# Performance work log

Measured on AMD Instinct MI355X. Metric: run time of the kernel, lower is better.

## Reference

```python
import jax, jax.numpy as jnp
import numpy as np

N = 50000      # nodes
E = 800000     # edges (before self-loops)
IN_C = 128
H_C = 64
HEADS = 4
OUT_C = 16
NEG_SLOPE = 0.2  # PyG GATConv default


def setup_inputs() -> dict:
    key = jax.random.key(0)
    ks = jax.random.split(key, 11)
    x = jax.random.normal(ks[0], (N, IN_C), dtype=jnp.float32)
    edge_index = jax.random.randint(ks[1], (2, E), 0, N, dtype=jnp.int64)
    def p(k, shape, fan_in):
        return jax.random.normal(k, shape, dtype=jnp.float32) / np.sqrt(fan_in)
    return {
        "x": x,
        "edge_index": edge_index,
        "W1": p(ks[2], (IN_C, HEADS * H_C), IN_C),
        "att_src1": p(ks[3], (HEADS, H_C), H_C),
        "att_dst1": p(ks[4], (HEADS, H_C), H_C),
        "b1": jnp.zeros((HEADS * H_C,), dtype=jnp.float32),
        "W2": p(ks[5], (HEADS * H_C, OUT_C), HEADS * H_C),
        "att_src2": p(ks[6], (1, OUT_C), OUT_C),
        "att_dst2": p(ks[7], (1, OUT_C), OUT_C),
        "b2": jnp.zeros((OUT_C,), dtype=jnp.float32),
    }


def _gat_layer(x, src, dst, W, a_src, a_dst, b, concat):
    n = x.shape[0]
    heads, C = a_src.shape
    h = (x @ W).reshape(n, heads, C)                      # [N,H,C]
    al_s = jnp.einsum('nhc,hc->nh', h, a_src)             # [N,H]
    al_d = jnp.einsum('nhc,hc->nh', h, a_dst)
    e = jax.nn.leaky_relu(al_s[src] + al_d[dst], NEG_SLOPE)  # [E,H]
    # segment softmax over destination neighborhoods
    m = jax.lax.stop_gradient(jax.ops.segment_max(e, dst, num_segments=n))
    p = jnp.exp(e - m[dst])
    denom = jax.ops.segment_sum(p, dst, num_segments=n)
    alpha = p / (denom[dst] + 1e-16)                      # [E,H]
    out = jax.ops.segment_sum(alpha[:, :, None] * h[src], dst, num_segments=n)  # [N,H,C]
    out = out.reshape(n, heads * C) if concat else out.mean(axis=1)
    return out + b


def reference(x, edge_index, W1, att_src1, att_dst1, b1, W2, att_src2, att_dst2, b2):
    # PyG GATConv add_self_loops=True
    loop = jnp.arange(N, dtype=edge_index.dtype)
    src = jnp.concatenate([edge_index[0], loop])
    dst = jnp.concatenate([edge_index[1], loop])
    h = jax.nn.relu(_gat_layer(x, src, dst, W1, att_src1, att_dst1, b1, True))
    out = _gat_layer(h, src, dst, W2, att_src2, att_dst2, b2, False)
    return jax.nn.log_softmax(out, axis=-1)
```

## Files before the change

kernel.cpp:

```cpp
#include <hip/hip_runtime.h>
#include <hip/hip_fp16.h>
#include <cstdint>
#include <cstddef>

#define NEG 0.2f

typedef _Float16 f16x8 __attribute__((ext_vector_type(8)));
typedef float f32x4 __attribute__((ext_vector_type(4)));

__device__ inline float lrelu(float v) { return v > 0.f ? v : NEG * v; }

__global__ void k_pre(const int* __restrict__ ei, int* __restrict__ deg,
                      const float* __restrict__ W1, f16x8* __restrict__ W1s,
                      int E, int ET) {
  int e = blockIdx.x * 256 + threadIdx.x;
  if (e < ET) {
    int d = (e < E) ? ei[E + e] : e - E;
    atomicAdd(&deg[d], 1);
  }
  if (blockIdx.x < 16) {
    int tau = blockIdx.x * 256 + threadIdx.x;
    int l = tau & 63, ct = (tau >> 6) & 15, ks = tau >> 10;
    int col = ct * 16 + (l & 15);
    f16x8 v;
    #pragma unroll
    for (int j = 0; j < 8; j++) {
      int k = ks * 32 + ((j < 4) ? ((l >> 4) * 4 + j) : (16 + (l >> 4) * 4 + (j - 4)));
      v[j] = (_Float16)W1[k * 256 + col];
    }
    W1s[tau] = v;
  }
}

__global__ __launch_bounds__(256) void k_gemm1f(const float* __restrict__ X,
                                                const f16x8* __restrict__ W1s,
                                                const float* __restrict__ as1,
                                                const float* __restrict__ ad1,
                                                __half* __restrict__ H16,
                                                float* __restrict__ als,
                                                float* __restrict__ ald, int N) {
  __shared__ __align__(16) char lds[32768];
  _Float16* A = (_Float16*)lds;
  int t = threadIdx.x;
  int rb = blockIdx.x * 64;
  int l = t & 63, wv = t >> 6;

  #pragma unroll
  for (int i = 0; i < 8; i++) {
    int idx = i * 256 + t;
    int row = idx >> 5, q = idx & 31;
    int gr = rb + row; if (gr >= N) gr = N - 1;
    float4 xv = *(const float4*)(X + (size_t)gr * 128 + q * 4);
    int ks = q >> 3, g = q & 3, hg = (q >> 2) & 1;
    int gran = (ks * 4 + g) ^ (row & 7);
    _Float16* dst = A + row * 128 + gran * 8 + hg * 4;
    dst[0] = (_Float16)xv.x; dst[1] = (_Float16)xv.y;
    dst[2] = (_Float16)xv.z; dst[3] = (_Float16)xv.w;
  }
  __syncthreads();

  f32x4 acc[4][4] = {};
  #pragma unroll
  for (int ks = 0; ks < 4; ks++) {
    f16x8 bfr[4];
    #pragma unroll
    for (int ct = 0; ct < 4; ct++)
      bfr[ct] = W1s[(ks * 16 + wv * 4 + ct) * 64 + l];
    #pragma unroll
    for (int rt = 0; rt < 4; rt++) {
      int row = rt * 16 + (l & 15);
      int gran = (ks * 4 + (l >> 4)) ^ (row & 7);
      f16x8 afr = *(const f16x8*)(A + row * 128 + gran * 8);
      #pragma unroll
      for (int ct = 0; ct < 4; ct++)
        acc[rt][ct] = __builtin_amdgcn_mfma_f32_16x16x32_f16(afr, bfr[ct], acc[rt][ct], 0, 0, 0);
    }
  }

  float asv[4], adv[4];
  #pragma unroll
  for (int ct = 0; ct < 4; ct++) {
    asv[ct] = as1[wv * 64 + ct * 16 + (l & 15)];
    adv[ct] = ad1[wv * 64 + ct * 16 + (l & 15)];
  }
  #pragma unroll
  for (int rt = 0; rt < 4; rt++) {
    #pragma unroll
    for (int j = 0; j < 4; j++) {
      float ps = 0.f, pd = 0.f;
      #pragma unroll
      for (int ct = 0; ct < 4; ct++) {
        ps += acc[rt][ct][j] * asv[ct];
        pd += acc[rt][ct][j] * adv[ct];
      }
      ps += __shfl_xor(ps, 1); ps += __shfl_xor(ps, 2);
      ps += __shfl_xor(ps, 4); ps += __shfl_xor(ps, 8);
      pd += __shfl_xor(pd, 1); pd += __shfl_xor(pd, 2);
      pd += __shfl_xor(pd, 4); pd += __shfl_xor(pd, 8);
      if ((l & 15) == 0) {
        int gr = rb + rt * 16 + (l >> 4) * 4 + j;
        if (gr < N) { als[gr * 4 + wv] = ps; ald[gr * 4 + wv] = pd; }
      }
    }
  }

  __syncthreads();
  _Float16* HL = (_Float16*)lds;
  #pragma unroll
  for (int rt = 0; rt < 4; rt++) {
    #pragma unroll
    for (int j = 0; j < 4; j++) {
      int row = rt * 16 + (l >> 4) * 4 + j;
      #pragma unroll
      for (int ct = 0; ct < 4; ct++) {
        int col = wv * 64 + ct * 16 + (l & 15);
        int g2 = (col >> 3) ^ ((row & 7) << 2);
        HL[row * 256 + g2 * 8 + (col & 7)] = (_Float16)acc[rt][ct][j];
      }
    }
  }
  __syncthreads();
  #pragma unroll
  for (int i = 0; i < 8; i++) {
    int idx = i * 256 + t;
    int row = idx >> 5, g = idx & 31;
    int g2 = g ^ ((row & 7) << 2);
    f32x4 v = *(const f32x4*)(HL + row * 256 + g2 * 8);
    int gr = rb + row;
    if (gr < N) *(f32x4*)((char*)H16 + (size_t)gr * 512 + g * 16) = v;
  }
}

__global__ __launch_bounds__(256) void k_scan_partial(const int* __restrict__ deg,
                                                      int* __restrict__ bsum, int N) {
  __shared__ int sd[256];
  int t = threadIdx.x;
  int base = blockIdx.x * 1024 + t * 4;
  int s = 0;
  #pragma unroll
  for (int j = 0; j < 4; j++) { int i = base + j; s += (i < N) ? deg[i] : 0; }
  sd[t] = s;
  __syncthreads();
  for (int o = 128; o > 0; o >>= 1) {
    if (t < o) sd[t] += sd[t + o];
    __syncthreads();
  }
  if (t == 0) bsum[blockIdx.x] = sd[0];
}

__global__ __launch_bounds__(256) void k_scan_final(const int* __restrict__ deg,
                                                    const int* __restrict__ bsum,
                                                    int* __restrict__ offsets,
                                                    int* __restrict__ cursor,
                                                    int N, int NB) {
  __shared__ int sd[256];
  __shared__ int boffs;
  int b = blockIdx.x, t = threadIdx.x;
  if (t == 0) {
    int r = 0;
    for (int i = 0; i < b; i++) r += bsum[i];
    boffs = r;
  }
  int base = b * 1024 + t * 4;
  int v[4]; int s = 0;
  #pragma unroll
  for (int j = 0; j < 4; j++) { int i = base + j; v[j] = (i < N) ? deg[i] : 0; s += v[j]; }
  int my = s;
  sd[t] = s;
  __syncthreads();
  for (int o = 1; o < 256; o <<= 1) {
    int add = (t >= o) ? sd[t - o] : 0;
    __syncthreads();
    sd[t] += add;
    __syncthreads();
  }
  int run = sd[t] - my + boffs;
  #pragma unroll
  for (int j = 0; j < 4; j++) {
    int i = base + j;
    if (i < N) { offsets[i] = run; cursor[i] = run; run += v[j]; }
  }
  if (b == NB - 1 && t == 255) offsets[N] = boffs + sd[255];
}

__global__ void k_fill(const int* __restrict__ ei, int* __restrict__ cursor,
                       int* __restrict__ csr_src, int E, int ET) {
  int e = blockIdx.x * 256 + threadIdx.x;
  if (e >= ET) return;
  int s, d;
  if (e < E) { s = ei[e]; d = ei[E + e]; } else { s = d = e - E; }
  int pos = atomicAdd(&cursor[d], 1);
  csr_src[pos] = s;
}

__device__ inline void acc8(float4 v, float p, float* a, float& s) {
  __half2 h0 = __builtin_bit_cast(__half2, v.x);
  __half2 h1 = __builtin_bit_cast(__half2, v.y);
  __half2 h2 = __builtin_bit_cast(__half2, v.z);
  __half2 h3 = __builtin_bit_cast(__half2, v.w);
  float2 f0 = __half22float2(h0), f1 = __half22float2(h1);
  float2 f2 = __half22float2(h2), f3 = __half22float2(h3);
  a[0] += p * f0.x; a[1] += p * f0.y; a[2] += p * f1.x; a[3] += p * f1.y;
  a[4] += p * f2.x; a[5] += p * f2.y; a[6] += p * f3.x; a[7] += p * f3.y;
  s += p;
}

__global__ __launch_bounds__(256) void k_agg1(const int* __restrict__ off,
                                              const int* __restrict__ csr_src,
                                              const float* __restrict__ als1,
                                              const float* __restrict__ ald1,
                                              const float4* __restrict__ H16,
                                              const float* __restrict__ b1,
                                              __half* __restrict__ H2, int N) {
  int t = threadIdx.x;
  int n = blockIdx.x * 4 + (t >> 6);
  if (n >= N) return;
  int lane = t & 31;
  int half = (t >> 5) & 1;
  int g = lane >> 3;
  float aldn = ald1[n * 4 + g];
  int st0 = off[n], en0 = off[n + 1];
  int mid = (st0 + en0 + 1) >> 1;
  int st = half ? mid : st0;
  int en = half ? en0 : mid;
  float a[8] = {0.f, 0.f, 0.f, 0.f, 0.f, 0.f, 0.f, 0.f};
  float s = 0.f;
  int i = st;
  for (; i + 4 <= en; i += 4) {
    int s0 = csr_src[i], s1 = csr_src[i + 1], s2 = csr_src[i + 2], s3 = csr_src[i + 3];
    float p0 = __expf(lrelu(als1[s0 * 4 + g] + aldn));
    float p1 = __expf(lrelu(als1[s1 * 4 + g] + aldn));
    float p2 = __expf(lrelu(als1[s2 * 4 + g] + aldn));
    float p3 = __expf(lrelu(als1[s3 * 4 + g] + aldn));
    float4 v0 = H16[(size_t)s0 * 32 + lane];
    float4 v1 = H16[(size_t)s1 * 32 + lane];
    float4 v2 = H16[(size_t)s2 * 32 + lane];
    float4 v3 = H16[(size_t)s3 * 32 + lane];
    acc8(v0, p0, a, s); acc8(v1, p1, a, s); acc8(v2, p2, a, s); acc8(v3, p3, a, s);
  }
  for (; i < en; i++) {
    int s0 = csr_src[i];
    float p0 = __expf(lrelu(als1[s0 * 4 + g] + aldn));
    float4 v0 = H16[(size_t)s0 * 32 + lane];
    acc8(v0, p0, a, s);
  }
  #pragma unroll
  for (int j = 0; j < 8; j++) a[j] += __shfl_xor(a[j], 32);
  s += __shfl_xor(s, 32);
  if (half == 0) {
    float inv = 1.f / (s + 1e-16f);
    int c0 = lane * 8;
    float4 bb0 = *(const float4*)(b1 + c0);
    float4 bb1 = *(const float4*)(b1 + c0 + 4);
    f16x8 o;
    o[0] = (_Float16)fmaxf(a[0] * inv + bb0.x, 0.f);
    o[1] = (_Float16)fmaxf(a[1] * inv + bb0.y, 0.f);
    o[2] = (_Float16)fmaxf(a[2] * inv + bb0.z, 0.f);
    o[3] = (_Float16)fmaxf(a[3] * inv + bb0.w, 0.f);
    o[4] = (_Float16)fmaxf(a[4] * inv + bb1.x, 0.f);
    o[5] = (_Float16)fmaxf(a[5] * inv + bb1.y, 0.f);
    o[6] = (_Float16)fmaxf(a[6] * inv + bb1.z, 0.f);
    o[7] = (_Float16)fmaxf(a[7] * inv + bb1.w, 0.f);
    *(f16x8*)((char*)H2 + (size_t)n * 512 + lane * 16) = o;
  }
}

__global__ __launch_bounds__(256) void k_gemm2(const __half* __restrict__ H2,
                                               const float* __restrict__ W2,
                                               const float* __restrict__ as2,
                                               const float* __restrict__ ad2,
                                               float* __restrict__ Z,
                                               float* __restrict__ als2,
                                               float* __restrict__ ald2, int N) {
  __shared__ float w2s[4096];
  int t = threadIdx.x;
  for (int i = t; i < 4096; i += 256) w2s[i] = W2[i];
  __syncthreads();
  int n = blockIdx.x * 16 + (t >> 4);
  int c = t & 15;
  if (n >= N) return;
  const f16x8* hp = (const f16x8*)((const char*)H2 + (size_t)n * 512);
  float acc = 0.f;
  #pragma unroll 8
  for (int kb = 0; kb < 32; kb++) {
    f16x8 hv = hp[kb];
    #pragma unroll
    for (int j = 0; j < 8; j++)
      acc += (float)hv[j] * w2s[(kb * 8 + j) * 16 + c];
  }
  Z[(size_t)n * 16 + c] = acc;
  float ps = acc * as2[c], pd = acc * ad2[c];
  #pragma unroll
  for (int o = 8; o > 0; o >>= 1) {
    ps += __shfl_down(ps, o, 16);
    pd += __shfl_down(pd, o, 16);
  }
  if (c == 0) { als2[n] = ps; ald2[n] = pd; }
}

__global__ __launch_bounds__(256) void k_agg2x(const int* __restrict__ off,
                                               const int* __restrict__ csr_src,
                                               const float* __restrict__ als2,
                                               const float* __restrict__ ald2,
                                               const float* __restrict__ Z,
                                               const float* __restrict__ b2,
                                               float* __restrict__ out, int N) {
  int t = threadIdx.x;
  int n = blockIdx.x * 8 + (t >> 5);
  if (n >= N) return;
  int c = t & 15;
  int half = (t >> 4) & 1;
  float aldn = ald2[n];
  int st0 = off[n], en0 = off[n + 1];
  int mid = (st0 + en0 + 1) >> 1;
  int st = half ? mid : st0;
  int en = half ? en0 : mid;
  float s = 0.f, acc = 0.f;
  int i = st;
  for (; i + 4 <= en; i += 4) {
    int s0 = csr_src[i], s1 = csr_src[i + 1], s2 = csr_src[i + 2], s3 = csr_src[i + 3];
    float p0 = __expf(lrelu(als2[s0] + aldn));
    float p1 = __expf(lrelu(als2[s1] + aldn));
    float p2 = __expf(lrelu(als2[s2] + aldn));
    float p3 = __expf(lrelu(als2[s3] + aldn));
    float z0 = Z[(size_t)s0 * 16 + c];
    float z1 = Z[(size_t)s1 * 16 + c];
    float z2 = Z[(size_t)s2 * 16 + c];
    float z3 = Z[(size_t)s3 * 16 + c];
    acc += p0 * z0 + p1 * z1 + p2 * z2 + p3 * z3;
    s += p0 + p1 + p2 + p3;
  }
  for (; i < en; i++) {
    int s0 = csr_src[i];
    float p0 = __expf(lrelu(als2[s0] + aldn));
    acc += p0 * Z[(size_t)s0 * 16 + c];
    s += p0;
  }
  acc += __shfl_xor(acc, 16);
  s += __shfl_xor(s, 16);
  if (half == 0) {
    float v = acc / (s + 1e-16f) + b2[c];
    float mx = v;
    #pragma unroll
    for (int o = 8; o > 0; o >>= 1) mx = fmaxf(mx, __shfl_xor(mx, o, 16));
    float ex = __expf(v - mx);
    float sm = ex;
    #pragma unroll
    for (int o = 8; o > 0; o >>= 1) sm += __shfl_xor(sm, o, 16);
    out[(size_t)n * 16 + c] = v - mx - logf(sm);
  }
}

extern "C" void kernel_launch(void* const* d_in, const int* in_sizes, int n_in,
                              void* d_out, int out_size, void* d_ws, size_t ws_size,
                              hipStream_t stream) {
  const float* x   = (const float*)d_in[0];
  const int*   ei  = (const int*)d_in[1];
  const float* W1  = (const float*)d_in[2];
  const float* as1 = (const float*)d_in[3];
  const float* ad1 = (const float*)d_in[4];
  const float* b1  = (const float*)d_in[5];
  const float* W2  = (const float*)d_in[6];
  const float* as2 = (const float*)d_in[7];
  const float* ad2 = (const float*)d_in[8];
  const float* b2  = (const float*)d_in[9];
  float* out = (float*)d_out;

  int N  = in_sizes[0] / 128;
  int E  = in_sizes[1] / 2;
  int ET = E + N;
  int NB = (N + 1023) / 1024;

  char* w = (char*)d_ws;
  size_t off_b = 0;
  auto alloc = [&](size_t bytes) -> char* {
    size_t start = (off_b + 255) & ~(size_t)255;
    off_b = start + bytes;
    return w + start;
  };
  __half*   h16  = (__half*)alloc((size_t)N * 256 * 2);
  __half*   h2   = (__half*)alloc((size_t)N * 256 * 2);
  f16x8*    w1s  = (f16x8*)alloc((size_t)4096 * 16);
  float*    als1 = (float*)alloc((size_t)N * 4 * 4);
  float*    ald1 = (float*)alloc((size_t)N * 4 * 4);
  int*      deg  = (int*)alloc((size_t)N * 4);
  int*      offs = (int*)alloc((size_t)(N + 1) * 4);
  int*      cur  = (int*)alloc((size_t)N * 4);
  int*      bsum = (int*)alloc((size_t)NB * 4);
  int*      csrs = (int*)alloc((size_t)ET * 4);
  float*    z    = (float*)alloc((size_t)N * 16 * 4);
  float*    als2 = (float*)alloc((size_t)N * 4);
  float*    ald2 = (float*)alloc((size_t)N * 4);

  hipMemsetAsync(deg, 0, (size_t)N * 4, stream);

  k_pre<<<(ET + 255) / 256, 256, 0, stream>>>(ei, deg, W1, w1s, E, ET);
  k_gemm1f<<<(N + 63) / 64, 256, 0, stream>>>(x, w1s, as1, ad1, h16, als1, ald1, N);
  k_scan_partial<<<NB, 256, 0, stream>>>(deg, bsum, N);
  k_scan_final<<<NB, 256, 0, stream>>>(deg, bsum, offs, cur, N, NB);
  k_fill<<<(ET + 255) / 256, 256, 0, stream>>>(ei, cur, csrs, E, ET);
  k_agg1<<<(N + 3) / 4, 256, 0, stream>>>(offs, csrs, als1, ald1, (const float4*)h16, b1, h2, N);
  k_gemm2<<<(N + 15) / 16, 256, 0, stream>>>(h2, W2, as2, ad2, z, als2, ald2, N);
  k_agg2x<<<(N + 7) / 8, 256, 0, stream>>>(offs, csrs, als2, ald2, z, b2, out, N);
}
```

Baseline: 233.1 us.

## Fuse CSR build phases into one cooperative kernel with grid syncs

Replaces the memset, degree count, W1 swizzle, two scan kernels and the CSR fill with a single cooperative kernel of 1024 blocks that uses grid-wide syncs between phases. This removes several kernel launches and their gaps. In exchange it adds grid barriers, runs a serial block-offset prefix on one thread, and uses a fixed grid size that must fit co-resident on the device, so phases no longer overlap with the GEMM.

```diff
diff --git a/kernel.cpp b/kernel.cpp
--- a/kernel.cpp
+++ b/kernel.cpp
@@ -1,8 +1,11 @@
 #include <hip/hip_runtime.h>
 #include <hip/hip_fp16.h>
+#include <hip/hip_cooperative_groups.h>
 #include <cstdint>
 #include <cstddef>
 
+namespace cg = cooperative_groups;
+
 #define NEG 0.2f
 
 typedef _Float16 f16x8 __attribute__((ext_vector_type(8)));
@@ -10,16 +13,30 @@
 
 __device__ inline float lrelu(float v) { return v > 0.f ? v : NEG * v; }
 
-__global__ void k_pre(const int* __restrict__ ei, int* __restrict__ deg,
-                      const float* __restrict__ W1, f16x8* __restrict__ W1s,
-                      int E, int ET) {
-  int e = blockIdx.x * 256 + threadIdx.x;
-  if (e < ET) {
+__global__ __launch_bounds__(256) void k_csr(const int* __restrict__ ei,
+                                             int* __restrict__ deg,
+                                             const float* __restrict__ W1,
+                                             f16x8* __restrict__ W1s,
+                                             int* __restrict__ bsum,
+                                             int* __restrict__ boff,
+                                             int* __restrict__ offs,
+                                             int* __restrict__ cur,
+                                             int* __restrict__ csrs,
+                                             int E, int ET, int N, int NCH) {
+  cg::grid_group grid = cg::this_grid();
+  __shared__ int sd[256];
+  int t = threadIdx.x;
+  int gid = blockIdx.x * 256 + t;
+  int gsz = gridDim.x * 256;
+
+  for (int i = gid; i < N; i += gsz) deg[i] = 0;
+  grid.sync();
+
+  for (int e = gid; e < ET; e += gsz) {
     int d = (e < E) ? ei[E + e] : e - E;
     atomicAdd(&deg[d], 1);
   }
-  if (blockIdx.x < 16) {
-    int tau = blockIdx.x * 256 + threadIdx.x;
+  for (int tau = gid; tau < 4096; tau += gsz) {
     int l = tau & 63, ct = (tau >> 6) & 15, ks = tau >> 10;
     int col = ct * 16 + (l & 15);
     f16x8 v;
@@ -29,6 +46,59 @@
       v[j] = (_Float16)W1[k * 256 + col];
     }
     W1s[tau] = v;
+  }
+  grid.sync();
+
+  if (blockIdx.x < (unsigned)NCH) {
+    int base = blockIdx.x * 1024 + t * 4;
+    int s = 0;
+    #pragma unroll
+    for (int j = 0; j < 4; j++) { int i = base + j; s += (i < N) ? deg[i] : 0; }
+    sd[t] = s;
+    __syncthreads();
+    for (int o = 128; o > 0; o >>= 1) {
+      if (t < o) sd[t] += sd[t + o];
+      __syncthreads();
+    }
+    if (t == 0) bsum[blockIdx.x] = sd[0];
+  }
+  grid.sync();
+
+  if (gid == 0) {
+    int run = 0;
+    for (int i = 0; i < NCH; i++) { boff[i] = run; run += bsum[i]; }
+    offs[N] = run;
+  }
+  grid.sync();
+
+  if (blockIdx.x < (unsigned)NCH) {
+    int base = blockIdx.x * 1024 + t * 4;
+    int v[4]; int s = 0;
+    #pragma unroll
+    for (int j = 0; j < 4; j++) { int i = base + j; v[j] = (i < N) ? deg[i] : 0; s += v[j]; }
+    int my = s;
+    sd[t] = s;
+    __syncthreads();
+    for (int o = 1; o < 256; o <<= 1) {
+      int add = (t >= o) ? sd[t - o] : 0;
+      __syncthreads();
+      sd[t] += add;
+      __syncthreads();
+    }
+    int run = sd[t] - my + boff[blockIdx.x];
+    #pragma unroll
+    for (int j = 0; j < 4; j++) {
+      int i = base + j;
+      if (i < N) { offs[i] = run; cur[i] = run; run += v[j]; }
+    }
+  }
+  grid.sync();
+
+  for (int e = gid; e < ET; e += gsz) {
+    int s, d;
+    if (e < E) { s = ei[e]; d = ei[E + e]; } else { s = d = e - E; }
+    int pos = atomicAdd(&cur[d], 1);
+    csrs[pos] = s;
   }
 }
 
@@ -129,68 +199,6 @@
     int gr = rb + row;
     if (gr < N) *(f32x4*)((char*)H16 + (size_t)gr * 512 + g * 16) = v;
   }
-}
-
-__global__ __launch_bounds__(256) void k_scan_partial(const int* __restrict__ deg,
-                                                      int* __restrict__ bsum, int N) {
-  __shared__ int sd[256];
-  int t = threadIdx.x;
-  int base = blockIdx.x * 1024 + t * 4;
-  int s = 0;
-  #pragma unroll
-  for (int j = 0; j < 4; j++) { int i = base + j; s += (i < N) ? deg[i] : 0; }
-  sd[t] = s;
-  __syncthreads();
-  for (int o = 128; o > 0; o >>= 1) {
-    if (t < o) sd[t] += sd[t + o];
-    __syncthreads();
-  }
-  if (t == 0) bsum[blockIdx.x] = sd[0];
-}
-
-__global__ __launch_bounds__(256) void k_scan_final(const int* __restrict__ deg,
-                                                    const int* __restrict__ bsum,
-                                                    int* __restrict__ offsets,
-                                                    int* __restrict__ cursor,
-                                                    int N, int NB) {
-  __shared__ int sd[256];
-  __shared__ int boffs;
-  int b = blockIdx.x, t = threadIdx.x;
-  if (t == 0) {
-    int r = 0;
-    for (int i = 0; i < b; i++) r += bsum[i];
-    boffs = r;
-  }
-  int base = b * 1024 + t * 4;
-  int v[4]; int s = 0;
-  #pragma unroll
-  for (int j = 0; j < 4; j++) { int i = base + j; v[j] = (i < N) ? deg[i] : 0; s += v[j]; }
-  int my = s;
-  sd[t] = s;
-  __syncthreads();
-  for (int o = 1; o < 256; o <<= 1) {
-    int add = (t >= o) ? sd[t - o] : 0;
-    __syncthreads();
-    sd[t] += add;
-    __syncthreads();
-  }
-  int run = sd[t] - my + boffs;
-  #pragma unroll
-  for (int j = 0; j < 4; j++) {
-    int i = base + j;
-    if (i < N) { offsets[i] = run; cursor[i] = run; run += v[j]; }
-  }
-  if (b == NB - 1 && t == 255) offsets[N] = boffs + sd[255];
-}
-
-__global__ void k_fill(const int* __restrict__ ei, int* __restrict__ cursor,
-                       int* __restrict__ csr_src, int E, int ET) {
-  int e = blockIdx.x * 256 + threadIdx.x;
-  if (e >= ET) return;
-  int s, d;
-  if (e < E) { s = ei[e]; d = ei[E + e]; } else { s = d = e - E; }
-  int pos = atomicAdd(&cursor[d], 1);
-  csr_src[pos] = s;
 }
 
 __device__ inline void acc8(float4 v, float p, float* a, float& s) {
@@ -369,7 +377,7 @@
   int N  = in_sizes[0] / 128;
   int E  = in_sizes[1] / 2;
   int ET = E + N;
-  int NB = (N + 1023) / 1024;
+  int NCH = (N + 1023) / 1024;
 
   char* w = (char*)d_ws;
   size_t off_b = 0;
@@ -386,19 +394,20 @@
   int*      deg  = (int*)alloc((size_t)N * 4);
   int*      offs = (int*)alloc((size_t)(N + 1) * 4);
   int*      cur  = (int*)alloc((size_t)N * 4);
-  int*      bsum = (int*)alloc((size_t)NB * 4);
+  int*      bsum = (int*)alloc((size_t)NCH * 4);
+  int*      boff = (int*)alloc((size_t)NCH * 4);
   int*      csrs = (int*)alloc((size_t)ET * 4);
   float*    z    = (float*)alloc((size_t)N * 16 * 4);
   float*    als2 = (float*)alloc((size_t)N * 4);
   float*    ald2 = (float*)alloc((size_t)N * 4);
 
-  hipMemsetAsync(deg, 0, (size_t)N * 4, stream);
-
-  k_pre<<<(ET + 255) / 256, 256, 0, stream>>>(ei, deg, W1, w1s, E, ET);
+  {
+    void* args[] = {(void*)&ei, (void*)&deg, (void*)&W1, (void*)&w1s,
+                    (void*)&bsum, (void*)&boff, (void*)&offs, (void*)&cur,
+                    (void*)&csrs, (void*)&E, (void*)&ET, (void*)&N, (void*)&NCH};
+    hipLaunchCooperativeKernel((void*)k_csr, dim3(1024), dim3(256), args, 0, stream);
+  }
   k_gemm1f<<<(N + 63) / 64, 256, 0, stream>>>(x, w1s, as1, ad1, h16, als1, ald1, N);
-  k_scan_partial<<<NB, 256, 0, stream>>>(deg, bsum, N);
-  k_scan_final<<<NB, 256, 0, stream>>>(deg, bsum, offs, cur, N, NB);
-  k_fill<<<(ET + 255) / 256, 256, 0, stream>>>(ei, cur, csrs, E, ET);
   k_agg1<<<(N + 3) / 4, 256, 0, stream>>>(offs, csrs, als1, ald1, (const float4*)h16, b1, h2, N);
   k_gemm2<<<(N + 15) / 16, 256, 0, stream>>>(h2, W2, as2, ad2, z, als2, ald2, N);
   k_agg2x<<<(N + 7) / 8, 256, 0, stream>>>(offs, csrs, als2, ald2, z, b2, out, N);
```

Result: slower. 699.4 us (+200.1%).

## Fuse layer-1 aggregation with layer-2 GEMM and fold scan partial into GEMM1

Applied to the files above, without the earlier changes.

The layer-1 aggregation now keeps each node's 256-wide ReLU output in LDS and immediately multiplies it by W2 in the same block, so the fp16 H2 intermediate no longer goes through global memory and the k_gemm2 launch is dropped. The scan-partial block sums move into the tail of k_gemm1f, removing one more launch. The cost is that every aggregation block (N/4 of them) now loads the full 16 KB W2 into LDS. Only 64 of 256 threads do the small GEMM, and the extra LDS use may lower occupancy of the gather-bound aggregation.

```diff
diff --git a/kernel.cpp b/kernel.cpp
--- a/kernel.cpp
+++ b/kernel.cpp
@@ -38,7 +38,10 @@
                                                 const float* __restrict__ ad1,
                                                 __half* __restrict__ H16,
                                                 float* __restrict__ als,
-                                                float* __restrict__ ald, int N) {
+                                                float* __restrict__ ald,
+                                                const int* __restrict__ deg,
+                                                int* __restrict__ bsum,
+                                                int N, int NB) {
   __shared__ __align__(16) char lds[32768];
   _Float16* A = (_Float16*)lds;
   int t = threadIdx.x;
@@ -129,23 +132,22 @@
     int gr = rb + row;
     if (gr < N) *(f32x4*)((char*)H16 + (size_t)gr * 512 + g * 16) = v;
   }
-}
-
-__global__ __launch_bounds__(256) void k_scan_partial(const int* __restrict__ deg,
-                                                      int* __restrict__ bsum, int N) {
-  __shared__ int sd[256];
-  int t = threadIdx.x;
-  int base = blockIdx.x * 1024 + t * 4;
-  int s = 0;
-  #pragma unroll
-  for (int j = 0; j < 4; j++) { int i = base + j; s += (i < N) ? deg[i] : 0; }
-  sd[t] = s;
-  __syncthreads();
-  for (int o = 128; o > 0; o >>= 1) {
-    if (t < o) sd[t] += sd[t + o];
+
+  if (blockIdx.x < (unsigned)NB) {
     __syncthreads();
-  }
-  if (t == 0) bsum[blockIdx.x] = sd[0];
+    int* sd = (int*)lds;
+    int base = blockIdx.x * 1024 + t * 4;
+    int s = 0;
+    #pragma unroll
+    for (int j = 0; j < 4; j++) { int i = base + j; s += (i < N) ? deg[i] : 0; }
+    sd[t] = s;
+    __syncthreads();
+    for (int o = 128; o > 0; o >>= 1) {
+      if (t < o) sd[t] += sd[t + o];
+      __syncthreads();
+    }
+    if (t == 0) bsum[blockIdx.x] = sd[0];
+  }
 }
 
 __global__ __launch_bounds__(256) void k_scan_final(const int* __restrict__ deg,
@@ -205,67 +207,12 @@
   s += p;
 }
 
-__global__ __launch_bounds__(256) void k_agg1(const int* __restrict__ off,
-                                              const int* __restrict__ csr_src,
-                                              const float* __restrict__ als1,
-                                              const float* __restrict__ ald1,
-                                              const float4* __restrict__ H16,
-                                              const float* __restrict__ b1,
-                                              __half* __restrict__ H2, int N) {
-  int t = threadIdx.x;
-  int n = blockIdx.x * 4 + (t >> 6);
-  if (n >= N) return;
-  int lane = t & 31;
-  int half = (t >> 5) & 1;
-  int g = lane >> 3;
-  float aldn = ald1[n * 4 + g];
-  int st0 = off[n], en0 = off[n + 1];
-  int mid = (st0 + en0 + 1) >> 1;
-  int st = half ? mid : st0;
-  int en = half ? en0 : mid;
-  float a[8] = {0.f, 0.f, 0.f, 0.f, 0.f, 0.f, 0.f, 0.f};
-  float s = 0.f;
-  int i = st;
-  for (; i + 4 <= en; i += 4) {
-    int s0 = csr_src[i], s1 = csr_src[i + 1], s2 = csr_src[i + 2], s3 = csr_src[i + 3];
-    float p0 = __expf(lrelu(als1[s0 * 4 + g] + aldn));
-    float p1 = __expf(lrelu(als1[s1 * 4 + g] + aldn));
-    float p2 = __expf(lrelu(als1[s2 * 4 + g] + aldn));
-    float p3 = __expf(lrelu(als1[s3 * 4 + g] + aldn));
-    float4 v0 = H16[(size_t)s0 * 32 + lane];
-    float4 v1 = H16[(size_t)s1 * 32 + lane];
-    float4 v2 = H16[(size_t)s2 * 32 + lane];
-    float4 v3 = H16[(size_t)s3 * 32 + lane];
-    acc8(v0, p0, a, s); acc8(v1, p1, a, s); acc8(v2, p2, a, s); acc8(v3, p3, a, s);
-  }
-  for (; i < en; i++) {
-    int s0 = csr_src[i];
-    float p0 = __expf(lrelu(als1[s0 * 4 + g] + aldn));
-    float4 v0 = H16[(size_t)s0 * 32 + lane];
-    acc8(v0, p0, a, s);
-  }
-  #pragma unroll
-  for (int j = 0; j < 8; j++) a[j] += __shfl_xor(a[j], 32);
-  s += __shfl_xor(s, 32);
-  if (half == 0) {
-    float inv = 1.f / (s + 1e-16f);
-    int c0 = lane * 8;
-    float4 bb0 = *(const float4*)(b1 + c0);
-    float4 bb1 = *(const float4*)(b1 + c0 + 4);
-    f16x8 o;
-    o[0] = (_Float16)fmaxf(a[0] * inv + bb0.x, 0.f);
-    o[1] = (_Float16)fmaxf(a[1] * inv + bb0.y, 0.f);
-    o[2] = (_Float16)fmaxf(a[2] * inv + bb0.z, 0.f);
-    o[3] = (_Float16)fmaxf(a[3] * inv + bb0.w, 0.f);
-    o[4] = (_Float16)fmaxf(a[4] * inv + bb1.x, 0.f);
-    o[5] = (_Float16)fmaxf(a[5] * inv + bb1.y, 0.f);
-    o[6] = (_Float16)fmaxf(a[6] * inv + bb1.z, 0.f);
-    o[7] = (_Float16)fmaxf(a[7] * inv + bb1.w, 0.f);
-    *(f16x8*)((char*)H2 + (size_t)n * 512 + lane * 16) = o;
-  }
-}
-
-__global__ __launch_bounds__(256) void k_gemm2(const __half* __restrict__ H2,
+__global__ __launch_bounds__(256) void k_agg1z(const int* __restrict__ off,
+                                               const int* __restrict__ csr_src,
+                                               const float* __restrict__ als1,
+                                               const float* __restrict__ ald1,
+                                               const float4* __restrict__ H16,
+                                               const float* __restrict__ b1,
                                                const float* __restrict__ W2,
                                                const float* __restrict__ as2,
                                                const float* __restrict__ ad2,
@@ -273,29 +220,77 @@
                                                float* __restrict__ als2,
                                                float* __restrict__ ald2, int N) {
   __shared__ float w2s[4096];
+  __shared__ __align__(16) float h2L[4][260];
   int t = threadIdx.x;
   for (int i = t; i < 4096; i += 256) w2s[i] = W2[i];
-  __syncthreads();
-  int n = blockIdx.x * 16 + (t >> 4);
-  int c = t & 15;
-  if (n >= N) return;
-  const f16x8* hp = (const f16x8*)((const char*)H2 + (size_t)n * 512);
-  float acc = 0.f;
-  #pragma unroll 8
-  for (int kb = 0; kb < 32; kb++) {
-    f16x8 hv = hp[kb];
-    #pragma unroll
-    for (int j = 0; j < 8; j++)
-      acc += (float)hv[j] * w2s[(kb * 8 + j) * 16 + c];
-  }
-  Z[(size_t)n * 16 + c] = acc;
-  float ps = acc * as2[c], pd = acc * ad2[c];
-  #pragma unroll
-  for (int o = 8; o > 0; o >>= 1) {
-    ps += __shfl_down(ps, o, 16);
-    pd += __shfl_down(pd, o, 16);
-  }
-  if (c == 0) { als2[n] = ps; ald2[n] = pd; }
+  int wv = t >> 6;
+  int n = blockIdx.x * 4 + wv;
+  int lane = t & 31;
+  int half = (t >> 5) & 1;
+  int g = lane >> 3;
+  if (n < N) {
+    float aldn = ald1[n * 4 + g];
+    int st0 = off[n], en0 = off[n + 1];
+    int mid = (st0 + en0 + 1) >> 1;
+    int st = half ? mid : st0;
+    int en = half ? en0 : mid;
+    float a[8] = {0.f, 0.f, 0.f, 0.f, 0.f, 0.f, 0.f, 0.f};
+    float s = 0.f;
+    int i = st;
+    for (; i + 4 <= en; i += 4) {
+      int s0 = csr_src[i], s1 = csr_src[i + 1], s2 = csr_src[i + 2], s3 = csr_src[i + 3];
+      float p0 = __expf(lrelu(als1[s0 * 4 + g] + aldn));
+      float p1 = __expf(lrelu(als1[s1 * 4 + g] + aldn));
+      float p2 = __expf(lrelu(als1[s2 * 4 + g] + aldn));
+      float p3 = __expf(lrelu(als1[s3 * 4 + g] + aldn));
+      float4 v0 = H16[(size_t)s0 * 32 + lane];
+      float4 v1 = H16[(size_t)s1 * 32 + lane];
+      float4 v2 = H16[(size_t)s2 * 32 + lane];
+      float4 v3 = H16[(size_t)s3 * 32 + lane];
+      acc8(v0, p0, a, s); acc8(v1, p1, a, s); acc8(v2, p2, a, s); acc8(v3, p3, a, s);
+    }
+    for (; i < en; i++) {
+      int s0 = csr_src[i];
+      float p0 = __expf(lrelu(als1[s0 * 4 + g] + aldn));
+      float4 v0 = H16[(size_t)s0 * 32 + lane];
+      acc8(v0, p0, a, s);
+    }
+    #pragma unroll
+    for (int j = 0; j < 8; j++) a[j] += __shfl_xor(a[j], 32);
+    s += __shfl_xor(s, 32);
+    if (half == 0) {
+      float inv = 1.f / (s + 1e-16f);
+      int c0 = lane * 8;
+      #pragma unroll
+      for (int j = 0; j < 8; j++)
+        h2L[wv][c0 + j] = fmaxf(a[j] * inv + b1[c0 + j], 0.f);
+    }
+  }
+  __syncthreads();
+  if (t < 64) {
+    int nl = t >> 4;
+    int n2 = blockIdx.x * 4 + nl;
+    if (n2 < N) {
+      int c = t & 15;
+      float acc = 0.f;
+      #pragma unroll 8
+      for (int k = 0; k < 256; k += 4) {
+        float4 hv = *(const float4*)(&h2L[nl][k]);
+        acc += hv.x * w2s[(k + 0) * 16 + c];
+        acc += hv.y * w2s[(k + 1) * 16 + c];
+        acc += hv.z * w2s[(k + 2) * 16 + c];
+        acc += hv.w * w2s[(k + 3) * 16 + c];
+      }
+      Z[(size_t)n2 * 16 + c] = acc;
+      float ps = acc * as2[c], pd = acc * ad2[c];
+      #pragma unroll
+      for (int o = 8; o > 0; o >>= 1) {
+        ps += __shfl_down(ps, o, 16);
+        pd += __shfl_down(pd, o, 16);
+      }
+      if (c == 0) { als2[n2] = ps; ald2[n2] = pd; }
+    }
+  }
 }
 
 __global__ __launch_bounds__(256) void k_agg2x(const int* __restrict__ off,
@@ -379,7 +374,6 @@
     return w + start;
   };
   __half*   h16  = (__half*)alloc((size_t)N * 256 * 2);
-  __half*   h2   = (__half*)alloc((size_t)N * 256 * 2);
   f16x8*    w1s  = (f16x8*)alloc((size_t)4096 * 16);
   float*    als1 = (float*)alloc((size_t)N * 4 * 4);
   float*    ald1 = (float*)alloc((size_t)N * 4 * 4);
@@ -395,11 +389,11 @@
   hipMemsetAsync(deg, 0, (size_t)N * 4, stream);
 
   k_pre<<<(ET + 255) / 256, 256, 0, stream>>>(ei, deg, W1, w1s, E, ET);
-  k_gemm1f<<<(N + 63) / 64, 256, 0, stream>>>(x, w1s, as1, ad1, h16, als1, ald1, N);
-  k_scan_partial<<<NB, 256, 0, stream>>>(deg, bsum, N);
+  k_gemm1f<<<(N + 63) / 64, 256, 0, stream>>>(x, w1s, as1, ad1, h16, als1, ald1,
+                                              deg, bsum, N, NB);
   k_scan_final<<<NB, 256, 0, stream>>>(deg, bsum, offs, cur, N, NB);
   k_fill<<<(ET + 255) / 256, 256, 0, stream>>>(ei, cur, csrs, E, ET);
-  k_agg1<<<(N + 3) / 4, 256, 0, stream>>>(offs, csrs, als1, ald1, (const float4*)h16, b1, h2, N);
-  k_gemm2<<<(N + 15) / 16, 256, 0, stream>>>(h2, W2, as2, ad2, z, als2, ald2, N);
+  k_agg1z<<<(N + 3) / 4, 256, 0, stream>>>(offs, csrs, als1, ald1, (const float4*)h16,
+                                           b1, W2, as2, ad2, z, als2, ald2, N);
   k_agg2x<<<(N + 7) / 8, 256, 0, stream>>>(offs, csrs, als2, ald2, z, b2, out, N);
 }
```

Result: faster. 228.0 us (-2.2%).
